# Kernel optimization log

Measured on AMD Instinct MI355X. Metric: run time of the kernel, lower is better.

The kernel has to match this reference:

```python
import jax, jax.numpy as jnp
import numpy as np

N, E, D = 100000, 1600000, 128


def setup_inputs() -> dict:
    key = jax.random.key(0)
    ks = jax.random.split(key, 10)
    x = jax.random.normal(ks[0], (N, D), dtype=jnp.float32)
    edge_index = jax.random.randint(ks[1], (2, E), 0, N, dtype=jnp.int64)
    edge_weight = jax.random.uniform(ks[2], (E,), dtype=jnp.float32)
    s = 1.0 / np.sqrt(D)
    # PyG GraphConv params per layer: lin_rel (weight+bias), lin_root (weight, no bias)
    Wr0 = jax.random.uniform(ks[3], (D, D), jnp.float32, -s, s)
    br0 = jax.random.uniform(ks[4], (D,), jnp.float32, -s, s)
    Ws0 = jax.random.uniform(ks[5], (D, D), jnp.float32, -s, s)
    Wr1 = jax.random.uniform(ks[6], (D, D), jnp.float32, -s, s)
    br1 = jax.random.uniform(ks[7], (D,), jnp.float32, -s, s)
    Ws1 = jax.random.uniform(ks[8], (D, D), jnp.float32, -s, s)
    return {"x": x, "edge_index": edge_index, "edge_weight": edge_weight,
            "Wr0": Wr0, "br0": br0, "Ws0": Ws0,
            "Wr1": Wr1, "br1": br1, "Ws1": Ws1}


def _graph_conv(h, src, dst, Wr, br, Ws, ew=None):
    # message: gather source-node features (optionally scaled by edge weight)
    m = h[src]                                   # [E, D]
    if ew is not None:
        m = m * ew[:, None]
    agg = jax.ops.segment_sum(m, dst, num_segments=h.shape[0])  # [N, D] aggr='add'
    return agg @ Wr + br + h @ Ws                # lin_rel(agg) + lin_root(h)


def reference(x, edge_index, edge_weight, Wr0, br0, Ws0, Wr1, br1, Ws1):
    src, dst = edge_index[0], edge_index[1]
    h = jax.nn.relu(_graph_conv(x, src, dst, Wr0, br0, Ws0, edge_weight))
    h = jax.nn.relu(_graph_conv(h, src, dst, Wr1, br1, Ws1))
    return h
```

## Files before the change

### kernel.cpp

```cpp
#include <hip/hip_runtime.h>
#include <hip/hip_bf16.h>

#ifndef D_FEAT
#define D_FEAT 128
#endif

#define SLOTS 40
#define OVF_CAP 8192

typedef __attribute__((ext_vector_type(8))) short bf16x8;
typedef __attribute__((ext_vector_type(4))) float f32x4;
typedef unsigned long long u64;

__device__ __forceinline__ unsigned short f2bf(float f) {
    union { float f; unsigned u; } v; v.f = f;
    unsigned r = v.u + 0x7FFF + ((v.u >> 16) & 1);
    return (unsigned short)(r >> 16);
}
__device__ __forceinline__ float bf2f_lo(unsigned u) {
    union { unsigned u; float f; } v; v.u = u << 16; return v.f;
}
__device__ __forceinline__ float bf2f_hi(unsigned u) {
    union { unsigned u; float f; } v; v.u = u & 0xFFFF0000u; return v.f;
}

__global__ void scatter_ell(const int* __restrict__ src, const int* __restrict__ dst,
                            const float* __restrict__ ew, int E, int Q, int N,
                            int* __restrict__ pos, unsigned* __restrict__ ell,
                            int* __restrict__ ovf_cnt, int4* __restrict__ ovf) {
    const int p = blockIdx.x & 7;
    const int sub = blockIdx.x >> 3;
    const int nsub = gridDim.x >> 3;
    const int lo = p * Q;
    const int hi = min(lo + Q, N);
    for (int i = sub * 256 + threadIdx.x; i < E; i += nsub * 256) {
        const int d = dst[i];
        if (d >= lo && d < hi) {
            const int slot = atomicAdd(&pos[d], 1);
            if (slot < SLOTS) {
                const unsigned w12 = min(4095u, (unsigned)__float2int_rn(ew[i] * 4095.f));
                ell[(size_t)d * SLOTS + slot] = (unsigned)src[i] | (w12 << 20);
            } else {
                const int o = atomicAdd(ovf_cnt, 1);
                if (o < OVF_CAP)
                    ovf[o] = make_int4(src[i], d, __float_as_int(ew[i]), 0);
            }
        }
    }
}

template <bool WEIGHTED>
__global__ void ovf_fixup(const unsigned short* __restrict__ AX,
                          const int* __restrict__ ovf_cnt,
                          const int4* __restrict__ ovf,
                          unsigned short* __restrict__ AXagg) {
    const int n = min(*ovf_cnt, OVF_CAP);
    const int lane = threadIdx.x;
    for (int e = 0; e < n; ++e) {
        const int4 r = ovf[e];
        const float w = WEIGHTED ? __int_as_float(r.z) : 1.f;
        const unsigned u = *reinterpret_cast<const unsigned*>(
            AX + (size_t)(unsigned)r.x * 256 + 128 + lane * 2);
        unsigned* pa = reinterpret_cast<unsigned*>(
            AXagg + (size_t)r.y * 256 + lane * 2);
        const unsigned cur = *pa;
        const float ax = bf2f_lo(cur) + w * bf2f_lo(u);
        const float ay = bf2f_hi(cur) + w * bf2f_hi(u);
        *pa = (unsigned)f2bf(ax) | ((unsigned)f2bf(ay) << 16);
    }
}

__device__ __forceinline__ void pack_W_body(const float* __restrict__ Wr,
                                            const float* __restrict__ Ws,
                                            unsigned short* __restrict__ Wp,
                                            int t) {
    const int lane = t & 63;
    const int ct = (t >> 6) & 7;
    const int ks = t >> 9;
    const int col = ct * 16 + (lane & 15);
    const int kbase = ks * 32 + (lane >> 4) * 8;
    unsigned short v[8];
#pragma unroll
    for (int j = 0; j < 8; ++j) {
        const int k = kbase + j;
        const float w = (k < 128) ? Wr[(size_t)k * 128 + col]
                                  : Ws[(size_t)(k - 128) * 128 + col];
        v[j] = f2bf(w);
    }
    *reinterpret_cast<uint4*>(Wp + (size_t)t * 8) = *reinterpret_cast<uint4*>(v);
}

__global__ void prep_kernel(const float* __restrict__ x,
                            unsigned short* __restrict__ AX, int N, int nconv,
                            const float* __restrict__ Wr0, const float* __restrict__ Ws0,
                            unsigned short* __restrict__ Wp0,
                            const float* __restrict__ Wr1, const float* __restrict__ Ws1,
                            unsigned short* __restrict__ Wp1) {
    const int b = blockIdx.x;
    if (b < nconv) {
        const int i = b * 256 + threadIdx.x;
        if (i >= N * 32) return;
        const int row = i >> 5;
        const int c4 = (i & 31) * 4;
        float4 v = *reinterpret_cast<const float4*>(x + (size_t)row * 128 + c4);
        unsigned lo = (unsigned)f2bf(v.x) | ((unsigned)f2bf(v.y) << 16);
        unsigned hi = (unsigned)f2bf(v.z) | ((unsigned)f2bf(v.w) << 16);
        *reinterpret_cast<uint2*>(AX + (size_t)row * 256 + 128 + c4) = make_uint2(lo, hi);
    } else if (b < nconv + 16) {
        pack_W_body(Wr0, Ws0, Wp0, (b - nconv) * 256 + threadIdx.x);
    } else {
        pack_W_body(Wr1, Ws1, Wp1, (b - nconv - 16) * 256 + threadIdx.x);
    }
}

template <bool WEIGHTED>
__global__ void __launch_bounds__(256)
gather_ell(const unsigned short* __restrict__ AX,
           const int* __restrict__ pos,
           const unsigned* __restrict__ ell,
           unsigned short* __restrict__ AXagg,
           int N) {
    const int node = blockIdx.x * 4 + (threadIdx.x >> 6);
    const int lane = threadIdx.x & 63;
    if (node >= N) return;
    const int g = lane >> 4;
    const int c = lane & 15;

    const int deg = min(pos[node], SLOTS);
    const unsigned* ebase = ell + (size_t)node * SLOTS;

    float acc[8];
#pragma unroll
    for (int j = 0; j < 8; ++j) acc[j] = 0.f;

    auto body = [&](int i) {
        const unsigned r = ebase[i];
        const float w = WEIGHTED ? (float)(r >> 20) * (1.f / 4095.f) : 1.f;
        const uint4 v = *reinterpret_cast<const uint4*>(
            AX + (size_t)(r & 0xFFFFF) * 256 + 128 + c * 8);
        acc[0] += w * bf2f_lo(v.x); acc[1] += w * bf2f_hi(v.x);
        acc[2] += w * bf2f_lo(v.y); acc[3] += w * bf2f_hi(v.y);
        acc[4] += w * bf2f_lo(v.z); acc[5] += w * bf2f_hi(v.z);
        acc[6] += w * bf2f_lo(v.w); acc[7] += w * bf2f_hi(v.w);
    };

    int i = g;
    for (; i + 12 < deg; i += 16) { body(i); body(i + 4); body(i + 8); body(i + 12); }
    for (; i < deg; i += 4) body(i);

#pragma unroll
    for (int j = 0; j < 8; ++j) {
        acc[j] += __shfl_xor(acc[j], 16);
        acc[j] += __shfl_xor(acc[j], 32);
    }

    if (lane < 16) {
        uint4 o;
        o.x = (unsigned)f2bf(acc[0]) | ((unsigned)f2bf(acc[1]) << 16);
        o.y = (unsigned)f2bf(acc[2]) | ((unsigned)f2bf(acc[3]) << 16);
        o.z = (unsigned)f2bf(acc[4]) | ((unsigned)f2bf(acc[5]) << 16);
        o.w = (unsigned)f2bf(acc[6]) | ((unsigned)f2bf(acc[7]) << 16);
        *reinterpret_cast<uint4*>(AXagg + (size_t)node * 256 + c * 8) = o;
    }
}

template <bool TO_BF16>
__global__ void __launch_bounds__(256)
gemm_mfma(const unsigned short* __restrict__ AX,
          const unsigned short* __restrict__ Wp,
          const float* __restrict__ br,
          float* __restrict__ out,
          unsigned short* __restrict__ AXh,
          int N) {
    const int tid = threadIdx.x;
    const int wave = tid >> 6;
    const int lane = tid & 63;
    const int r0 = blockIdx.x * 128 + wave * 32;
    const int lk = (lane >> 4) * 8;

    int ra = r0 + (lane & 15);
    int rb = ra + 16;
    if (ra >= N) ra = N - 1;
    if (rb >= N) rb = N - 1;
    const unsigned short* pa = AX + (size_t)ra * 256 + lk;
    const unsigned short* pb = AX + (size_t)rb * 256 + lk;
    const unsigned short* pw = Wp + (size_t)lane * 8;

    f32x4 acc[2][8];
#pragma unroll
    for (int rt = 0; rt < 2; ++rt)
#pragma unroll
        for (int ct = 0; ct < 8; ++ct)
            acc[rt][ct] = (f32x4){0.f, 0.f, 0.f, 0.f};

#pragma unroll
    for (int ks = 0; ks < 8; ++ks) {
        const bf16x8 a0 = *reinterpret_cast<const bf16x8*>(pa + ks * 32);
        const bf16x8 a1 = *reinterpret_cast<const bf16x8*>(pb + ks * 32);
#pragma unroll
        for (int ct = 0; ct < 8; ++ct) {
            const bf16x8 b = *reinterpret_cast<const bf16x8*>(pw + (((ks << 3) + ct) << 9));
            acc[0][ct] = __builtin_amdgcn_mfma_f32_16x16x32_bf16(a0, b, acc[0][ct], 0, 0, 0);
            acc[1][ct] = __builtin_amdgcn_mfma_f32_16x16x32_bf16(a1, b, acc[1][ct], 0, 0, 0);
        }
    }

    const int crow = (lane >> 4) * 4;
    const int ccol = lane & 15;
#pragma unroll
    for (int ct = 0; ct < 8; ++ct) {
        const int col = ct * 16 + ccol;
        const float bias = br[col];
#pragma unroll
        for (int rt = 0; rt < 2; ++rt) {
#pragma unroll
            for (int reg = 0; reg < 4; ++reg) {
                const int row = r0 + rt * 16 + crow + reg;
                if (row >= N) continue;
                const float v = fmaxf(acc[rt][ct][reg] + bias, 0.f);
                if (TO_BF16) {
                    AXh[(size_t)row * 256 + 128 + col] = f2bf(v);
                } else {
                    out[(size_t)row * 128 + col] = v;
                }
            }
        }
    }
}

extern "C" void kernel_launch(void* const* d_in, const int* in_sizes, int n_in,
                              void* d_out, int out_size, void* d_ws, size_t ws_size,
                              hipStream_t stream) {
    const float* x  = (const float*)d_in[0];
    const int*   ei = (const int*)d_in[1];
    const float* ew = (const float*)d_in[2];
    const float* Wr0 = (const float*)d_in[3];
    const float* br0 = (const float*)d_in[4];
    const float* Ws0 = (const float*)d_in[5];
    const float* Wr1 = (const float*)d_in[6];
    const float* br1 = (const float*)d_in[7];
    const float* Ws1 = (const float*)d_in[8];

    const int N = in_sizes[0] / D_FEAT;
    const int E = in_sizes[1] / 2;
    const int* src = ei;
    const int* dst = ei + E;
    const int Q = (N + 7) / 8;

    char* w = (char*)d_ws;
    auto carve = [&](size_t bytes) { char* p = w; w += (bytes + 15) & ~(size_t)15; return p; };
    unsigned short* AX  = (unsigned short*)carve((size_t)N * 256 * 2);
    unsigned short* Wp0 = (unsigned short*)carve(256 * 128 * 2);
    unsigned short* Wp1 = (unsigned short*)carve(256 * 128 * 2);
    int*      pos     = (int*)     carve((size_t)N * 4);
    int*      ovf_cnt = (int*)     carve(16);
    int4*     ovf     = (int4*)    carve((size_t)OVF_CAP * 16);
    unsigned* ell     = (unsigned*)carve((size_t)N * SLOTS * 4);

    float* out = (float*)d_out;

    const int nconv = (N * 32 + 255) / 256;
    const int gather_blocks = (N + 3) / 4;
    const int gemm_blocks = (N + 127) / 128;

    prep_kernel<<<nconv + 32, 256, 0, stream>>>(x, AX, N, nconv,
                                                Wr0, Ws0, Wp0, Wr1, Ws1, Wp1);

    hipMemsetAsync(pos, 0, (size_t)N * 4, stream);
    hipMemsetAsync(ovf_cnt, 0, 4, stream);
    scatter_ell<<<2048, 256, 0, stream>>>(src, dst, ew, E, Q, N, pos, ell, ovf_cnt, ovf);

    gather_ell<true><<<gather_blocks, 256, 0, stream>>>(AX, pos, ell, AX, N);
    ovf_fixup<true><<<1, 64, 0, stream>>>(AX, ovf_cnt, ovf, AX);
    gemm_mfma<true><<<gemm_blocks, 256, 0, stream>>>(AX, Wp0, br0, nullptr, AX, N);

    gather_ell<false><<<gather_blocks, 256, 0, stream>>>(AX, pos, ell, AX, N);
    ovf_fixup<false><<<1, 64, 0, stream>>>(AX, ovf_cnt, ovf, AX);
    gemm_mfma<false><<<gemm_blocks, 256, 0, stream>>>(AX, Wp1, br1, out, nullptr, N);
}
```

Before: 290.0 us.

## Bind ELL scatter partitions to XCC with dynamic work-stealing chunks

```diff
diff --git a/kernel.cpp b/kernel.cpp
--- a/kernel.cpp
+++ b/kernel.cpp
@@ -7,6 +7,7 @@
 
 #define SLOTS 40
 #define OVF_CAP 8192
+#define SCH 8192
 
 typedef __attribute__((ext_vector_type(8))) short bf16x8;
 typedef __attribute__((ext_vector_type(4))) float f32x4;
@@ -24,26 +25,42 @@
     union { unsigned u; float f; } v; v.u = u & 0xFFFF0000u; return v.f;
 }
 
-__global__ void scatter_ell(const int* __restrict__ src, const int* __restrict__ dst,
-                            const float* __restrict__ ew, int E, int Q, int N,
-                            int* __restrict__ pos, unsigned* __restrict__ ell,
-                            int* __restrict__ ovf_cnt, int4* __restrict__ ovf) {
-    const int p = blockIdx.x & 7;
-    const int sub = blockIdx.x >> 3;
-    const int nsub = gridDim.x >> 3;
-    const int lo = p * Q;
-    const int hi = min(lo + Q, N);
-    for (int i = sub * 256 + threadIdx.x; i < E; i += nsub * 256) {
-        const int d = dst[i];
-        if (d >= lo && d < hi) {
-            const int slot = atomicAdd(&pos[d], 1);
-            if (slot < SLOTS) {
-                const unsigned w12 = min(4095u, (unsigned)__float2int_rn(ew[i] * 4095.f));
-                ell[(size_t)d * SLOTS + slot] = (unsigned)src[i] | (w12 << 20);
-            } else {
-                const int o = atomicAdd(ovf_cnt, 1);
-                if (o < OVF_CAP)
-                    ovf[o] = make_int4(src[i], d, __float_as_int(ew[i]), 0);
+__global__ void __launch_bounds__(256)
+scatter_ell(const int* __restrict__ src, const int* __restrict__ dst,
+            const float* __restrict__ ew, int E, int Q, int N,
+            int* __restrict__ cursor,
+            int* __restrict__ pos, unsigned* __restrict__ ell,
+            int* __restrict__ ovf_cnt, int4* __restrict__ ovf) {
+    __shared__ int sbase;
+    unsigned xcc;
+    asm("s_getreg_b32 %0, hwreg(HW_REG_XCC_ID)" : "=s"(xcc));
+    const int p0 = (int)(xcc & 7);
+
+    for (int pp = 0; pp < 8; ++pp) {
+        const int p = (p0 + pp) & 7;
+        const int lo = p * Q;
+        const int hi = min(lo + Q, N);
+        for (;;) {
+            if (threadIdx.x == 0) sbase = atomicAdd(&cursor[p], SCH);
+            __syncthreads();
+            const int base = sbase;
+            __syncthreads();
+            if (base >= E) break;
+            const int lim = min(base + SCH, E);
+            for (int i = base + threadIdx.x; i < lim; i += 256) {
+                const int d = dst[i];
+                if (d >= lo && d < hi) {
+                    const int slot = atomicAdd(&pos[d], 1);
+                    if (slot < SLOTS) {
+                        const unsigned w12 =
+                            min(4095u, (unsigned)__float2int_rn(ew[i] * 4095.f));
+                        ell[(size_t)d * SLOTS + slot] = (unsigned)src[i] | (w12 << 20);
+                    } else {
+                        const int o = atomicAdd(ovf_cnt, 1);
+                        if (o < OVF_CAP)
+                            ovf[o] = make_int4(src[i], d, __float_as_int(ew[i]), 0);
+                    }
+                }
             }
         }
     }
@@ -254,6 +271,7 @@
     unsigned short* Wp1 = (unsigned short*)carve(256 * 128 * 2);
     int*      pos     = (int*)     carve((size_t)N * 4);
     int*      ovf_cnt = (int*)     carve(16);
+    int*      cursor  = (int*)     carve(8 * 4);
     int4*     ovf     = (int4*)    carve((size_t)OVF_CAP * 16);
     unsigned* ell     = (unsigned*)carve((size_t)N * SLOTS * 4);
 
@@ -268,7 +286,9 @@
 
     hipMemsetAsync(pos, 0, (size_t)N * 4, stream);
     hipMemsetAsync(ovf_cnt, 0, 4, stream);
-    scatter_ell<<<2048, 256, 0, stream>>>(src, dst, ew, E, Q, N, pos, ell, ovf_cnt, ovf);
+    hipMemsetAsync(cursor, 0, 8 * 4, stream);
+    scatter_ell<<<2048, 256, 0, stream>>>(src, dst, ew, E, Q, N, cursor,
+                                          pos, ell, ovf_cnt, ovf);
 
     gather_ell<true><<<gather_blocks, 256, 0, stream>>>(AX, pos, ell, AX, N);
     ovf_fixup<true><<<1, 64, 0, stream>>>(AX, ovf_cnt, ovf, AX);
```

Result: slower. 474.5 us (+63.6%).
